# Optimization experiments

Hardware: AMD Instinct MI355X
Metric: run time of the kernel (lower is better)

## Reference

```python
import jax, jax.numpy as jnp
import numpy as np

WIDTH = 2048
NUM_HEADS = 16
HEAD_DIM = WIDTH // NUM_HEADS  # 128
ROPE_DIMS = HEAD_DIM // 2      # 64, partial rotary
WINDOW = 512
ROPE_BASE = 10000.0
NEG_INF = -1e9


def apply_rope(x, dims, offset=0, base=ROPE_BASE):
    # x: [B, H, L, hd]; non-traditional (half-split) rotary on first `dims` dims.
    L = x.shape[2]
    half = dims // 2
    pos = (offset + jnp.arange(L)).astype(x.dtype)                     # [L]
    inv_freq = jnp.exp(-jnp.log(jnp.asarray(base, x.dtype)) * (jnp.arange(0, dims, 2).astype(x.dtype) / dims))  # [half]
    theta = pos[:, None] * inv_freq[None, :]                           # [L, half]
    cos = jnp.cos(theta)[None, None]                                   # [1,1,L,half]
    sin = jnp.sin(theta)[None, None]
    x1 = x[..., :half]
    x2 = x[..., half:dims]
    rest = x[..., dims:]
    rx1 = x1 * cos - x2 * sin
    rx2 = x1 * sin + x2 * cos
    return jnp.concatenate([rx1, rx2, rest], axis=-1)


def setup_inputs() -> dict:
    key = jax.random.key(0)
    ks = jax.random.split(key, 6)
    B, L, D, hd = 2, 2048, WIDTH, HEAD_DIM
    x = jax.random.normal(ks[0], (B, L, D), dtype=jnp.float32)
    Wq = jax.random.normal(ks[1], (D, D), dtype=jnp.float32) * 0.02
    Wk = jax.random.normal(ks[2], (D, hd), dtype=jnp.float32) * 0.02
    Wv = jax.random.normal(ks[3], (D, hd), dtype=jnp.float32) * 0.02
    Wo = jax.random.normal(ks[4], (D, D), dtype=jnp.float32) * 0.02
    bo = jax.random.normal(ks[5], (D,), dtype=jnp.float32) * 0.02
    return {"x": x, "Wq": Wq, "Wk": Wk, "Wv": Wv, "Wo": Wo, "bo": bo}


def reference(x, Wq, Wk, Wv, Wo, bo):
    B, L, D = x.shape
    H, hd = NUM_HEADS, HEAD_DIM
    scale = hd ** (-0.5)

    q = (x @ Wq).reshape(B, L, H, hd).transpose(0, 2, 1, 3)   # [B,H,L,hd]
    k = (x @ Wk).reshape(B, L, 1, hd).transpose(0, 2, 1, 3)   # [B,1,L,hd] (MQA)
    v = (x @ Wv).reshape(B, L, 1, hd).transpose(0, 2, 1, 3)

    q = apply_rope(q, ROPE_DIMS)
    k = apply_rope(k, ROPE_DIMS)

    # sliding-window causal mask: attend iff 0 <= i - j < WINDOW
    i = jnp.arange(L)[:, None]
    j = jnp.arange(L)[None, :]
    allowed = (i - j >= 0) & (i - j < WINDOW)                  # [L,L]
    mask = jnp.where(allowed, 0.0, NEG_INF).astype(x.dtype)

    scores = jnp.einsum("bhqd,bkd->bhqk", q, k[:, 0]) * scale  # [B,H,L,L]
    scores = scores + mask[None, None]
    attn = jax.nn.softmax(scores, axis=-1)
    out = jnp.einsum("bhqk,bkd->bhqd", attn, v[:, 0])          # [B,H,L,hd]
    out = out.transpose(0, 2, 1, 3).reshape(B, L, D)
    return out @ Wo + bo
```

## Files before the change

### kernel.cpp

```cpp
#include <hip/hip_runtime.h>
#include <hip/hip_bf16.h>
#include <stdint.h>


typedef float  f32x4  __attribute__((ext_vector_type(4)));
typedef __bf16 bf16x8 __attribute__((ext_vector_type(8)));

#define ASYNC_LD16(gp, lp)                                                     \
  __builtin_amdgcn_global_load_lds(                                            \
      (__attribute__((address_space(1))) void*)(gp),                           \
      (__attribute__((address_space(3))) void*)(lp), 16, 0, 0)

__global__ __launch_bounds__(256) void prep_all(
    const float* __restrict__ x, __hip_bfloat16* __restrict__ xb,
    const float* __restrict__ Wq, const float* __restrict__ Wk,
    const float* __restrict__ Wv, const float* __restrict__ Wo,
    __hip_bfloat16* __restrict__ wqkvT, __hip_bfloat16* __restrict__ woT) {
  __shared__ float t[32][33];
  int bid = blockIdx.x;
  if (bid < 8192) {
    const int i = bid * 256 + threadIdx.x;
    const float4 v = ((const float4*)x)[i];
    __align__(8) __hip_bfloat16 o[4] = {
        __float2bfloat16(v.x), __float2bfloat16(v.y),
        __float2bfloat16(v.z), __float2bfloat16(v.w)};
    *(uint2*)(xb + (size_t)i * 4) = *(uint2*)o;
    return;
  }
  bid -= 8192;
  const float* src;
  __hip_bfloat16* dst;
  int C, cb, rb;
  if (bid < 4096) {
    src = Wq; dst = wqkvT; C = 2048; cb = bid & 63; rb = bid >> 6;
  } else if (bid < 4352) {
    const int l = bid - 4096;
    src = Wk; dst = wqkvT + 2048ull * 2048; C = 128; cb = l & 3; rb = l >> 2;
  } else if (bid < 4608) {
    const int l = bid - 4352;
    src = Wv; dst = wqkvT + 2176ull * 2048; C = 128; cb = l & 3; rb = l >> 2;
  } else {
    const int l = bid - 4608;
    src = Wo; dst = woT; C = 2048; cb = l & 63; rb = l >> 6;
  }
  const int c0 = cb * 32, r0 = rb * 32;
  const int xx = threadIdx.x & 31, y = threadIdx.x >> 5;
#pragma unroll
  for (int i = 0; i < 32; i += 8)
    t[y + i][xx] = src[(size_t)(r0 + y + i) * C + c0 + xx];
  __syncthreads();
#pragma unroll
  for (int i = 0; i < 32; i += 8)
    dst[(size_t)(c0 + y + i) * 2048 + r0 + xx] = __float2bfloat16(t[xx][y + i]);
}

__device__ __forceinline__ void xcd_remap(int& bx, int& by) {
  const int nwg = gridDim.x * gridDim.y;
  const int flat = blockIdx.y * gridDim.x + blockIdx.x;
  const int cpx = nwg >> 3;
  const int nid = (flat & 7) * cpx + (flat >> 3);
  bx = nid % gridDim.x;
  by = nid / gridDim.x;
}

__device__ __forceinline__ void gemm_core_db(const __bf16* __restrict__ A,
                                             const __bf16* __restrict__ BT,
                                             int K, int m0, int n0, __bf16* As,
                                             __bf16* Bs, f32x4 (&acc)[2][4]) {
  const int tid = threadIdx.x;
  const int wave = tid >> 6;
  const int lane = tid & 63;
  const int wm = (wave & 3) * 32;
  const int wn = (wave >> 2) * 64;
  const int ln = lane & 15;
  const int quad = lane >> 4;
  const int rdoff = (quad ^ ((ln >> 1) & 3)) * 8;

  size_t goff[2];
  int ldsoff[2];
#pragma unroll
  for (int i = 0; i < 2; i++) {
    const int cidx = (wave * 2 + i) * 64 + lane;
    const int p = cidx >> 9;
    const int pidx = cidx & 511;
    const int row = pidx >> 2;
    const int cc = pidx & 3;
    const int cg = cc ^ ((row >> 1) & 3);
    goff[i] = (size_t)row * K + p * 32 + cg * 8;
    ldsoff[i] = (wave * 2 + i) * 512;
  }
  const __bf16* Abase = A + (size_t)m0 * K;
  const __bf16* Bbase = BT + (size_t)n0 * K;
  const int NT = K >> 6;

#pragma unroll
  for (int i = 0; i < 2; i++) ASYNC_LD16(Abase + goff[i], As + ldsoff[i]);
#pragma unroll
  for (int i = 0; i < 2; i++) ASYNC_LD16(Bbase + goff[i], Bs + ldsoff[i]);

  int cur = 0;
  for (int t = 0; t < NT; ++t) {
    __syncthreads();
    if (t + 1 < NT) {
      const int k0 = (t + 1) << 6;
      __bf16* an = As + ((cur ^ 1) << 13);
      __bf16* bn = Bs + ((cur ^ 1) << 13);
#pragma unroll
      for (int i = 0; i < 2; i++)
        ASYNC_LD16(Abase + k0 + goff[i], an + ldsoff[i]);
#pragma unroll
      for (int i = 0; i < 2; i++)
        ASYNC_LD16(Bbase + k0 + goff[i], bn + ldsoff[i]);
    }
    const __bf16* as_ = As + (cur << 13);
    const __bf16* bs_ = Bs + (cur << 13);
    bf16x8 af[2][2], bfv[4][2];
#pragma unroll
    for (int i = 0; i < 2; i++)
#pragma unroll
      for (int p = 0; p < 2; p++)
        af[i][p] =
            *(const bf16x8*)&as_[p * 4096 + (wm + i * 16 + ln) * 32 + rdoff];
#pragma unroll
    for (int j = 0; j < 4; j++)
#pragma unroll
      for (int p = 0; p < 2; p++)
        bfv[j][p] =
            *(const bf16x8*)&bs_[p * 4096 + (wn + j * 16 + ln) * 32 + rdoff];
#pragma unroll
    for (int p = 0; p < 2; p++)
#pragma unroll
      for (int i = 0; i < 2; i++)
#pragma unroll
        for (int j = 0; j < 4; j++)
          acc[i][j] = __builtin_amdgcn_mfma_f32_16x16x32_bf16(
              af[i][p], bfv[j][p], acc[i][j], 0, 0, 0);
    cur ^= 1;
  }
}

__global__ __launch_bounds__(512) void gemm_qkv(
    const __bf16* __restrict__ A, const __bf16* __restrict__ BT,
    __hip_bfloat16* __restrict__ qd, __hip_bfloat16* __restrict__ kd,
    __hip_bfloat16* __restrict__ vtd, int K) {
  __shared__ __align__(16) __bf16 As[2 * 8192];
  __shared__ __align__(16) __bf16 Bs[2 * 8192];
  int bx, by;
  xcd_remap(bx, by);
  const int m0 = by * 128;
  const int n0 = bx * 128;
  f32x4 acc[2][4];
  const f32x4 zero = {0.f, 0.f, 0.f, 0.f};
#pragma unroll
  for (int i = 0; i < 2; i++)
#pragma unroll
    for (int j = 0; j < 4; j++) acc[i][j] = zero;
  gemm_core_db(A, BT, K, m0, n0, As, Bs, acc);

  const int tid = threadIdx.x;
  const int wave = tid >> 6;
  const int lane = tid & 63;
  const int quad = lane >> 4;
  const int ln = lane & 15;
  const int wm = (wave & 3) * 32;
  const int wn = (wave >> 2) * 64;

  if (n0 == 2176) {
    const int bb = m0 >> 11;
    const int mloc = m0 & 2047;
#pragma unroll
    for (int i = 0; i < 2; i++) {
      const int rb = mloc + wm + i * 16 + quad * 4;
#pragma unroll
      for (int j = 0; j < 4; j++) {
        const int col = wn + j * 16 + ln;
        __align__(8) __hip_bfloat16 t4[4];
#pragma unroll
        for (int r = 0; r < 4; r++) t4[r] = __float2bfloat16(acc[i][j][r]);
        *(uint2*)(vtd + ((size_t)(bb * 128 + col)) * 2048 + rb) = *(uint2*)t4;
      }
    }
    return;
  }

  __hip_bfloat16* dst;
  int dstride, dcol;
  if (n0 < 2048) {
    dst = qd; dstride = 2048; dcol = n0;
  } else {
    dst = kd; dstride = 128; dcol = 0;
  }
  const bool dorope = (wn == 0);
  float invf0 = 0.f, invf1 = 0.f;
  if (dorope) {
    invf0 = expf(-0.28782313662425574f * (float)ln);
    invf1 = expf(-0.28782313662425574f * (float)(16 + ln));
  }

#pragma unroll
  for (int i = 0; i < 2; i++) {
#pragma unroll
    for (int r = 0; r < 4; r++) {
      const int row = m0 + wm + i * 16 + quad * 4 + r;
      float o0 = acc[i][0][r], o1 = acc[i][1][r];
      float o2 = acc[i][2][r], o3 = acc[i][3][r];
      if (dorope) {
        const float pos = (float)(row & 2047);
        float s0, c0, s1, c1;
        __sincosf(pos * invf0, &s0, &c0);
        __sincosf(pos * invf1, &s1, &c1);
        const float a0 = o0, b0 = o2, a1 = o1, b1 = o3;
        o0 = a0 * c0 - b0 * s0;
        o2 = a0 * s0 + b0 * c0;
        o1 = a1 * c1 - b1 * s1;
        o3 = a1 * s1 + b1 * c1;
      }
      __hip_bfloat16* rp = dst + (size_t)row * dstride + dcol + wn + ln;
      rp[0]  = __float2bfloat16(o0);
      rp[16] = __float2bfloat16(o1);
      rp[32] = __float2bfloat16(o2);
      rp[48] = __float2bfloat16(o3);
    }
  }
}

__global__ __launch_bounds__(512) void gemm_out(
    const __bf16* __restrict__ A, const __bf16* __restrict__ BT,
    float* __restrict__ C, const float* __restrict__ bias, int N, int K) {
  __shared__ __align__(16) __bf16 As[2 * 8192];
  __shared__ __align__(16) __bf16 Bs[2 * 8192];
  int bx, by;
  xcd_remap(bx, by);
  const int m0 = by * 128;
  const int n0 = bx * 128;
  f32x4 acc[2][4];
  const f32x4 zero = {0.f, 0.f, 0.f, 0.f};
#pragma unroll
  for (int i = 0; i < 2; i++)
#pragma unroll
    for (int j = 0; j < 4; j++) acc[i][j] = zero;
  gemm_core_db(A, BT, K, m0, n0, As, Bs, acc);

  const int tid = threadIdx.x;
  const int wave = tid >> 6;
  const int lane = tid & 63;
  const int wm = (wave & 3) * 32;
  const int wn = (wave >> 2) * 64;
  const int lrow = lane & 15;
#pragma unroll
  for (int j = 0; j < 4; j++) {
    const int col = n0 + wn + j * 16 + lrow;
    const float bv = bias[col];
#pragma unroll
    for (int i = 0; i < 2; i++) {
#pragma unroll
      for (int r = 0; r < 4; r++) {
        const int row = m0 + wm + i * 16 + (lane >> 4) * 4 + r;
        C[(size_t)row * N + col] = acc[i][j][r] + bv;
      }
    }
  }
}

__global__ __launch_bounds__(256) void attn_mfma(
    const __bf16* __restrict__ qb,
    const __bf16* __restrict__ kb,
    const __bf16* __restrict__ vtb,
    __hip_bfloat16* __restrict__ o)
{
  __shared__ __align__(16) __bf16 Ks[2][4][64 * 32];
  __shared__ __align__(16) __bf16 Vs[2][2][128 * 32];
  __shared__ __align__(16) __bf16 Ps[4][2][2][512];
  const int tid = threadIdx.x;
  const int wave = tid >> 6;
  const int lane = tid & 63;
  const int quad = lane >> 4;
  const int ln = lane & 15;
  const int bid = blockIdx.x;
  const int q0 = (bid & 15) * 128;
  const int h = (bid >> 4) & 15;
  const int b = bid >> 8;
  const int swr = (ln >> 1) & 3;
  const int rdoff = (quad ^ swr) * 8;

  bf16x8 qf[2][4];
#pragma unroll
  for (int g = 0; g < 2; g++) {
    const __bf16* qrow =
        qb + ((size_t)(b * 2048 + q0 + wave * 32 + g * 16 + ln)) * 2048 + h * 128;
#pragma unroll
    for (int ks = 0; ks < 4; ks++)
      qf[g][ks] = *(const bf16x8*)(qrow + ks * 32 + quad * 8);
  }

  f32x4 oacc[2][8];
  const f32x4 zero = {0.f, 0.f, 0.f, 0.f};
#pragma unroll
  for (int g = 0; g < 2; g++)
#pragma unroll
    for (int nb = 0; nb < 8; nb++) oacc[g][nb] = zero;
  float li[2][4] = {{0.f, 0.f, 0.f, 0.f}, {0.f, 0.f, 0.f, 0.f}};
  const float scale = 0.08838834764831845f;

  const __bf16* kbase = kb + (size_t)b * 2048 * 128;
  const __bf16* vbase = vtb + (size_t)b * 128 * 2048;

  const int key4 = lane >> 2, uu = lane & 3;
  const int sw = (key4 >> 1) & 3;

  auto stage_kv = [&](int t, int bufi) {
    const int jt = q0 - 512 + 64 * t;
#pragma unroll
    for (int i = 0; i < 4; ++i) {
      const int c = wave * 4 + i;
      const int ks = c & 3, keybase = (c >> 2) * 16;
      ASYNC_LD16(kbase + (size_t)(jt + keybase + key4) * 128 + ks * 32 +
                     (uu ^ sw) * 8,
                 &Ks[bufi][ks][keybase * 32]);
    }
#pragma unroll
    for (int i = 0; i < 4; ++i) {
      const int c = wave * 4 + i;
      const int p = c & 1, dbase = (c >> 1) * 16;
      ASYNC_LD16(vbase + (size_t)(dbase + key4) * 2048 + jt + p * 32 +
                     (uu ^ sw) * 8,
                 &Vs[bufi][p][dbase * 32]);
    }
  };

#define SOFTMAX_BODY(MASKED)                                                   \
  _Pragma("unroll") for (int g = 0; g < 2; g++)                                \
  _Pragma("unroll") for (int j = 0; j < 4; j++)                                \
  _Pragma("unroll") for (int r = 0; r < 4; r++) {                              \
    float v = sacc[g][j][r] * scale;                                           \
    if (MASKED) {                                                              \
      const int d0 = (wave * 32 + g * 16 + quad * 4 + r) - (j * 16 + ln);      \
      if (t <= 1 && d0 >= (t << 6)) v = -1e30f;                                \
      if (t >= 8 && d0 < ((t - 8) << 6)) v = -1e30f;                           \
    }                                                                          \
    v = fminf(v, 60.f);                                                        \
    const float p = __expf(v);                                                 \
    li[g][r] += p;                                                             \
    const int ch = (j & 1) * 2 + (ln >> 3);                                    \
    const int swp = (quad * 2 + (r >> 1)) & 3;                                 \
    Ps[wave][g][j >> 1][(quad * 4 + r) * 32 + (ch ^ swp) * 8 + (ln & 7)] =     \
        (__bf16)p;                                                             \
  }

  const int tstart = (q0 >= 512) ? 0 : (512 - q0) / 64;
  int cur = 0;
  stage_kv(tstart, 0);
  for (int t = tstart; t < 10; ++t) {
    __syncthreads();
    if (t + 1 < 10) stage_kv(t + 1, cur ^ 1);

    f32x4 sacc[2][4];
#pragma unroll
    for (int g = 0; g < 2; g++)
#pragma unroll
      for (int j = 0; j < 4; j++) sacc[g][j] = zero;
    __builtin_amdgcn_s_setprio(1);
#pragma unroll
    for (int j = 0; j < 4; j++)
#pragma unroll
      for (int ks = 0; ks < 4; ks++) {
        const bf16x8 kf =
            *(const bf16x8*)&Ks[cur][ks][(j * 16 + ln) * 32 + rdoff];
#pragma unroll
        for (int g = 0; g < 2; g++)
          sacc[g][j] = __builtin_amdgcn_mfma_f32_16x16x32_bf16(
              qf[g][ks], kf, sacc[g][j], 0, 0, 0);
      }
    __builtin_amdgcn_s_setprio(0);

    if (t <= 1 || t >= 8) {
      SOFTMAX_BODY(1)
    } else {
      SOFTMAX_BODY(0)
    }

    const bf16x8 pf00 = *(const bf16x8*)&Ps[wave][0][0][ln * 32 + rdoff];
    const bf16x8 pf01 = *(const bf16x8*)&Ps[wave][0][1][ln * 32 + rdoff];
    const bf16x8 pf10 = *(const bf16x8*)&Ps[wave][1][0][ln * 32 + rdoff];
    const bf16x8 pf11 = *(const bf16x8*)&Ps[wave][1][1][ln * 32 + rdoff];
    __builtin_amdgcn_s_setprio(1);
#pragma unroll
    for (int nb = 0; nb < 8; nb++) {
      const bf16x8 vf0 =
          *(const bf16x8*)&Vs[cur][0][(nb * 16 + ln) * 32 + rdoff];
      const bf16x8 vf1 =
          *(const bf16x8*)&Vs[cur][1][(nb * 16 + ln) * 32 + rdoff];
      oacc[0][nb] = __builtin_amdgcn_mfma_f32_16x16x32_bf16(pf00, vf0,
                                                            oacc[0][nb], 0, 0, 0);
      oacc[0][nb] = __builtin_amdgcn_mfma_f32_16x16x32_bf16(pf01, vf1,
                                                            oacc[0][nb], 0, 0, 0);
      oacc[1][nb] = __builtin_amdgcn_mfma_f32_16x16x32_bf16(pf10, vf0,
                                                            oacc[1][nb], 0, 0, 0);
      oacc[1][nb] = __builtin_amdgcn_mfma_f32_16x16x32_bf16(pf11, vf1,
                                                            oacc[1][nb], 0, 0, 0);
    }
    __builtin_amdgcn_s_setprio(0);
    cur ^= 1;
  }
#undef SOFTMAX_BODY

#pragma unroll
  for (int off = 1; off < 16; off <<= 1)
#pragma unroll
    for (int g = 0; g < 2; g++)
#pragma unroll
      for (int r = 0; r < 4; r++) li[g][r] += __shfl_xor(li[g][r], off);

#pragma unroll
  for (int g = 0; g < 2; g++) {
    __hip_bfloat16* obase =
        o + ((size_t)(b * 2048 + q0 + wave * 32 + g * 16 + quad * 4)) * 2048 +
        h * 128 + ln;
#pragma unroll
    for (int r = 0; r < 4; r++) {
      const float inv = 1.0f / li[g][r];
#pragma unroll
      for (int nb = 0; nb < 8; nb++)
        obase[(size_t)r * 2048 + nb * 16] = __float2bfloat16(oacc[g][nb][r] * inv);
    }
  }
}

extern "C" void kernel_launch(void* const* d_in, const int* in_sizes, int n_in,
                              void* d_out, int out_size, void* d_ws,
                              size_t ws_size, hipStream_t stream) {
  const float* x = (const float*)d_in[0];
  const float* Wq = (const float*)d_in[1];
  const float* Wk = (const float*)d_in[2];
  const float* Wv = (const float*)d_in[3];
  const float* Wo = (const float*)d_in[4];
  const float* bo = (const float*)d_in[5];
  float* out = (float*)d_out;

  char* w = (char*)d_ws;
  auto alloc = [&](size_t bytes) {
    void* p = (void*)w;
    w += (bytes + 255) & ~(size_t)255;
    return p;
  };
  __bf16* xb = (__bf16*)alloc(4096ull * 2048 * 2);
  __hip_bfloat16* wqkvT = (__hip_bfloat16*)alloc(2304ull * 2048 * 2);
  __hip_bfloat16* woT = (__hip_bfloat16*)alloc(2048ull * 2048 * 2);
  __hip_bfloat16* qbuf = (__hip_bfloat16*)alloc(4096ull * 2048 * 2);
  __hip_bfloat16* kbuf = (__hip_bfloat16*)alloc(4096ull * 128 * 2);
  __hip_bfloat16* vtb = (__hip_bfloat16*)alloc(4096ull * 128 * 2);
  __hip_bfloat16* attnb = (__hip_bfloat16*)xb;

  prep_all<<<16896, 256, 0, stream>>>(x, (__hip_bfloat16*)xb, Wq, Wk, Wv, Wo,
                                      wqkvT, woT);

  gemm_qkv<<<dim3(18, 32), 512, 0, stream>>>(xb, (const __bf16*)wqkvT, qbuf,
                                             kbuf, vtb, 2048);

  attn_mfma<<<512, 256, 0, stream>>>((const __bf16*)qbuf, (const __bf16*)kbuf,
                                     (const __bf16*)vtb, attnb);

  gemm_out<<<dim3(16, 32), 512, 0, stream>>>((const __bf16*)attnb,
                                             (const __bf16*)woT, out, bo, 2048,
                                             2048);
}
```

Baseline: 253.8 us.

## Shrink GEMM tiles to 64x128 with 256 threads and single-buffered LDS

Both projection GEMMs now use 64x128 tiles computed by 4 waves of 256 threads instead of 128x128 tiles with 8 waves, which doubles the grid size. The double-buffered async prefetch is replaced by a single buffer that loads, synchronizes, computes and synchronizes again on each K step. The aim is more blocks and lower LDS use per block for better occupancy and load balance across CUs. The cost is twice the re-reading of the B operand and the loss of load/compute overlap within a block.

```diff
diff --git a/kernel.cpp b/kernel.cpp
--- a/kernel.cpp
+++ b/kernel.cpp
@@ -63,91 +63,88 @@
   by = nid / gridDim.x;
 }
 
-__device__ __forceinline__ void gemm_core_db(const __bf16* __restrict__ A,
-                                             const __bf16* __restrict__ BT,
-                                             int K, int m0, int n0, __bf16* As,
-                                             __bf16* Bs, f32x4 (&acc)[2][4]) {
+__device__ __forceinline__ void gemm_core64(const __bf16* __restrict__ A,
+                                            const __bf16* __restrict__ BT,
+                                            int K, int m0, int n0, __bf16* As,
+                                            __bf16* Bs, f32x4 (&acc)[2][4]) {
   const int tid = threadIdx.x;
   const int wave = tid >> 6;
   const int lane = tid & 63;
-  const int wm = (wave & 3) * 32;
-  const int wn = (wave >> 2) * 64;
+  const int wm = (wave & 1) * 32;
+  const int wn = (wave >> 1) * 64;
   const int ln = lane & 15;
   const int quad = lane >> 4;
   const int rdoff = (quad ^ ((ln >> 1) & 3)) * 8;
 
-  size_t goff[2];
-  int ldsoff[2];
+  size_t goffA[2];
+  int ldsoffA[2];
 #pragma unroll
   for (int i = 0; i < 2; i++) {
     const int cidx = (wave * 2 + i) * 64 + lane;
+    const int p = cidx >> 8;
+    const int pidx = cidx & 255;
+    const int row = pidx >> 2;
+    const int cc = pidx & 3;
+    const int cg = cc ^ ((row >> 1) & 3);
+    goffA[i] = (size_t)row * K + p * 32 + cg * 8;
+    ldsoffA[i] = (wave * 2 + i) * 512;
+  }
+  size_t goffB[4];
+  int ldsoffB[4];
+#pragma unroll
+  for (int i = 0; i < 4; i++) {
+    const int cidx = (wave * 4 + i) * 64 + lane;
     const int p = cidx >> 9;
     const int pidx = cidx & 511;
     const int row = pidx >> 2;
     const int cc = pidx & 3;
     const int cg = cc ^ ((row >> 1) & 3);
-    goff[i] = (size_t)row * K + p * 32 + cg * 8;
-    ldsoff[i] = (wave * 2 + i) * 512;
+    goffB[i] = (size_t)row * K + p * 32 + cg * 8;
+    ldsoffB[i] = (wave * 4 + i) * 512;
   }
   const __bf16* Abase = A + (size_t)m0 * K;
   const __bf16* Bbase = BT + (size_t)n0 * K;
-  const int NT = K >> 6;
-
-#pragma unroll
-  for (int i = 0; i < 2; i++) ASYNC_LD16(Abase + goff[i], As + ldsoff[i]);
-#pragma unroll
-  for (int i = 0; i < 2; i++) ASYNC_LD16(Bbase + goff[i], Bs + ldsoff[i]);
-
-  int cur = 0;
-  for (int t = 0; t < NT; ++t) {
+
+  for (int k0 = 0; k0 < K; k0 += 64) {
+#pragma unroll
+    for (int i = 0; i < 2; i++)
+      ASYNC_LD16(Abase + k0 + goffA[i], As + ldsoffA[i]);
+#pragma unroll
+    for (int i = 0; i < 4; i++)
+      ASYNC_LD16(Bbase + k0 + goffB[i], Bs + ldsoffB[i]);
     __syncthreads();
-    if (t + 1 < NT) {
-      const int k0 = (t + 1) << 6;
-      __bf16* an = As + ((cur ^ 1) << 13);
-      __bf16* bn = Bs + ((cur ^ 1) << 13);
+    bf16x8 af[2][2], bf[4][2];
+#pragma unroll
+    for (int i = 0; i < 2; i++)
+#pragma unroll
+      for (int p = 0; p < 2; p++)
+        af[i][p] = *(const bf16x8*)&As[p * 2048 + (wm + i * 16 + ln) * 32 + rdoff];
+#pragma unroll
+    for (int j = 0; j < 4; j++)
+#pragma unroll
+      for (int p = 0; p < 2; p++)
+        bf[j][p] = *(const bf16x8*)&Bs[p * 4096 + (wn + j * 16 + ln) * 32 + rdoff];
+#pragma unroll
+    for (int p = 0; p < 2; p++)
 #pragma unroll
       for (int i = 0; i < 2; i++)
-        ASYNC_LD16(Abase + k0 + goff[i], an + ldsoff[i]);
-#pragma unroll
-      for (int i = 0; i < 2; i++)
-        ASYNC_LD16(Bbase + k0 + goff[i], bn + ldsoff[i]);
-    }
-    const __bf16* as_ = As + (cur << 13);
-    const __bf16* bs_ = Bs + (cur << 13);
-    bf16x8 af[2][2], bfv[4][2];
-#pragma unroll
-    for (int i = 0; i < 2; i++)
-#pragma unroll
-      for (int p = 0; p < 2; p++)
-        af[i][p] =
-            *(const bf16x8*)&as_[p * 4096 + (wm + i * 16 + ln) * 32 + rdoff];
-#pragma unroll
-    for (int j = 0; j < 4; j++)
-#pragma unroll
-      for (int p = 0; p < 2; p++)
-        bfv[j][p] =
-            *(const bf16x8*)&bs_[p * 4096 + (wn + j * 16 + ln) * 32 + rdoff];
-#pragma unroll
-    for (int p = 0; p < 2; p++)
-#pragma unroll
-      for (int i = 0; i < 2; i++)
 #pragma unroll
         for (int j = 0; j < 4; j++)
-          acc[i][j] = __builtin_amdgcn_mfma_f32_16x16x32_bf16(
-              af[i][p], bfv[j][p], acc[i][j], 0, 0, 0);
-    cur ^= 1;
-  }
-}
-
-__global__ __launch_bounds__(512) void gemm_qkv(
+          acc[i][j] = __builtin_amdgcn_mfma_f32_16x16x32_bf16(af[i][p], bf[j][p],
+                                                              acc[i][j], 0, 0, 0);
+    __syncthreads();
+  }
+}
+
+__global__ __launch_bounds__(256) void gemm_qkv(
     const __bf16* __restrict__ A, const __bf16* __restrict__ BT,
     __hip_bfloat16* __restrict__ qd, __hip_bfloat16* __restrict__ kd,
     __hip_bfloat16* __restrict__ vtd, int K) {
-  __shared__ __align__(16) __bf16 As[2 * 8192];
-  __shared__ __align__(16) __bf16 Bs[2 * 8192];
+  __shared__ __align__(16) __bf16 As[2 * 2048];
+  __shared__ __align__(16) __bf16 Bs[2 * 4096];
   int bx, by;
   xcd_remap(bx, by);
-  const int m0 = by * 128;
+  const int m0 = by * 64;
   const int n0 = bx * 128;
   f32x4 acc[2][4];
   const f32x4 zero = {0.f, 0.f, 0.f, 0.f};
@@ -155,15 +152,15 @@
   for (int i = 0; i < 2; i++)
 #pragma unroll
     for (int j = 0; j < 4; j++) acc[i][j] = zero;
-  gemm_core_db(A, BT, K, m0, n0, As, Bs, acc);
+  gemm_core64(A, BT, K, m0, n0, As, Bs, acc);
 
   const int tid = threadIdx.x;
   const int wave = tid >> 6;
   const int lane = tid & 63;
   const int quad = lane >> 4;
   const int ln = lane & 15;
-  const int wm = (wave & 3) * 32;
-  const int wn = (wave >> 2) * 64;
+  const int wm = (wave & 1) * 32;
+  const int wn = (wave >> 1) * 64;
 
   if (n0 == 2176) {
     const int bb = m0 >> 11;
@@ -224,14 +221,14 @@
   }
 }
 
-__global__ __launch_bounds__(512) void gemm_out(
+__global__ __launch_bounds__(256) void gemm_out(
     const __bf16* __restrict__ A, const __bf16* __restrict__ BT,
     float* __restrict__ C, const float* __restrict__ bias, int N, int K) {
-  __shared__ __align__(16) __bf16 As[2 * 8192];
-  __shared__ __align__(16) __bf16 Bs[2 * 8192];
+  __shared__ __align__(16) __bf16 As[2 * 2048];
+  __shared__ __align__(16) __bf16 Bs[2 * 4096];
   int bx, by;
   xcd_remap(bx, by);
-  const int m0 = by * 128;
+  const int m0 = by * 64;
   const int n0 = bx * 128;
   f32x4 acc[2][4];
   const f32x4 zero = {0.f, 0.f, 0.f, 0.f};
@@ -239,13 +236,13 @@
   for (int i = 0; i < 2; i++)
 #pragma unroll
     for (int j = 0; j < 4; j++) acc[i][j] = zero;
-  gemm_core_db(A, BT, K, m0, n0, As, Bs, acc);
+  gemm_core64(A, BT, K, m0, n0, As, Bs, acc);
 
   const int tid = threadIdx.x;
   const int wave = tid >> 6;
   const int lane = tid & 63;
-  const int wm = (wave & 3) * 32;
-  const int wn = (wave >> 2) * 64;
+  const int wm = (wave & 1) * 32;
+  const int wn = (wave >> 1) * 64;
   const int lrow = lane & 15;
 #pragma unroll
   for (int j = 0; j < 4; j++) {
@@ -454,13 +451,13 @@
   prep_all<<<16896, 256, 0, stream>>>(x, (__hip_bfloat16*)xb, Wq, Wk, Wv, Wo,
                                       wqkvT, woT);
 
-  gemm_qkv<<<dim3(18, 32), 512, 0, stream>>>(xb, (const __bf16*)wqkvT, qbuf,
+  gemm_qkv<<<dim3(18, 64), 256, 0, stream>>>(xb, (const __bf16*)wqkvT, qbuf,
                                              kbuf, vtb, 2048);
 
   attn_mfma<<<512, 256, 0, stream>>>((const __bf16*)qbuf, (const __bf16*)kbuf,
                                      (const __bf16*)vtb, attnb);
 
-  gemm_out<<<dim3(16, 32), 512, 0, stream>>>((const __bf16*)attnb,
+  gemm_out<<<dim3(16, 64), 256, 0, stream>>>((const __bf16*)attnb,
                                              (const __bf16*)woT, out, bo, 2048,
                                              2048);
 }
```

Result: no change. 249.7 us (-1.6%).
